# Optimization experiments

Measured on AMD Instinct MI355X. Metric: run time of the kernel, lower is better.

Reference implementation:

```python
import jax, jax.numpy as jnp
import numpy as np

N, IN, H, D, R, L, E, C = 100000, 128, 2, 64, 3, 2, 500000, 64
HID = H * D  # 128
EPS = 1e-5
NEG_SLOPE = 0.2


def setup_inputs() -> dict:
    key = jax.random.key(0)
    ks = jax.random.split(key, 11)
    s = 1.0 / np.sqrt(HID)
    return {
        "feat": jax.random.normal(ks[0], (N, IN), jnp.float32),
        "Ws": jax.random.normal(ks[1], (L, R, HID, HID), jnp.float32) * s,
        "als": jax.random.normal(ks[2], (L, R, H, D), jnp.float32) * s,
        "ars": jax.random.normal(ks[3], (L, R, H, D), jnp.float32) * s,
        "bs": jax.random.normal(ks[4], (L, R, HID), jnp.float32) * 0.01,
        "bn_w": jax.random.uniform(ks[5], (HID,), jnp.float32, 0.5, 1.5),
        "bn_b": jax.random.normal(ks[6], (HID,), jnp.float32) * 0.01,
        "clf_W": jax.random.normal(ks[7], (HID, C), jnp.float32) * s,
        "clf_b": jax.random.normal(ks[8], (C,), jnp.float32) * 0.01,
        "src": jax.random.randint(ks[9], (R, E), 0, N, jnp.int32),
        "dst": jax.random.randint(ks[10], (R, E), 0, N, jnp.int32),
    }


def _gat_rel(h, src, dst, W, al, ar, b):
    # DGL GATConv: feat [N,H,D]; e = leaky_relu(a_l.Wh_u + a_r.Wh_v);
    # alpha = softmax over in-edges of dst; out = scatter-sum(alpha*Wh_src) + bias
    feat = (h @ W).reshape(N, H, D)                     # [N,H,D]
    el = jnp.sum(feat * al, axis=-1)                    # [N,H]
    er = jnp.sum(feat * ar, axis=-1)                    # [N,H]
    e = jax.nn.leaky_relu(el[src] + er[dst], NEG_SLOPE) # [E,H]
    m = jax.ops.segment_max(e, dst, num_segments=N)     # [N,H]
    ex = jnp.exp(e - m[dst])
    ssum = jax.ops.segment_sum(ex, dst, num_segments=N)
    alpha = ex / ssum[dst]                              # [E,H]
    msg = feat[src] * alpha[:, :, None]                 # [E,H,D]
    out = jax.ops.segment_sum(msg, dst, num_segments=N) # [N,H,D]
    return out + b.reshape(1, H, D)


def reference(feat, Ws, als, ars, bs, bn_w, bn_b, clf_W, clf_b, src, dst):
    h = feat
    for l in range(L):
        acc = jnp.zeros((N, H, D), h.dtype)
        for r in range(R):  # HeteroGraphConv aggregate='sum' over relations
            acc = acc + _gat_rel(h, src[r], dst[r], Ws[l, r], als[l, r], ars[l, r], bs[l, r])
        h = jax.nn.relu(acc).reshape(N, HID)  # concat multihead agg
    # BatchNorm1d (training mode: batch stats, biased var) + Linear
    mu = jnp.mean(h, axis=0)
    var = jnp.var(h, axis=0)
    h = (h - mu) / jnp.sqrt(var + EPS) * bn_w + bn_b
    return h @ clf_W + clf_b
```

## Files before the change

kernel.cpp:

```cpp
#include <hip/hip_runtime.h>
#include <hip/hip_bf16.h>

#define N_NODES 100000
#define N_EDGES 500000
#define HID 128
#define NEG_SLOPE 0.2f
#define NB 98

typedef __attribute__((ext_vector_type(8))) short short8v;
typedef __attribute__((ext_vector_type(4))) short short4v;
typedef __attribute__((ext_vector_type(4))) float f32x4;

__device__ __forceinline__ short f2bf(float x) {
    union { float f; unsigned u; } v; v.f = x;
    unsigned r = v.u + 0x7fff + ((v.u >> 16) & 1);
    return (short)(r >> 16);
}
__device__ __forceinline__ float bflo(unsigned u) {
    union { unsigned x; float f; } c; c.x = u << 16; return c.f;
}
__device__ __forceinline__ float bfhi(unsigned u) {
    union { unsigned x; float f; } c; c.x = u & 0xffff0000u; return c.f;
}
__device__ __forceinline__ float bfs(short s) {
    union { unsigned x; float f; } c; c.x = ((unsigned)(unsigned short)s) << 16; return c.f;
}
__device__ __forceinline__ float asf(unsigned u) {
    union { unsigned x; float f; } c; c.x = u; return c.f;
}


__global__ __launch_bounds__(256) void k_bhist(const int* __restrict__ dst, int* __restrict__ bcnt) {
    int r = blockIdx.y, tid = threadIdx.x;
    int base = blockIdx.x * 4096;
    __shared__ int h[128];
    if (tid < 128) h[tid] = 0;
    __syncthreads();
    size_t eb = (size_t)r * N_EDGES;
    int lim = min(base + 4096, N_EDGES);
    for (int e = base + tid; e < lim; e += 256) atomicAdd(&h[dst[eb + e] >> 10], 1);
    __syncthreads();
    if (tid < NB && h[tid]) atomicAdd(&bcnt[r * NB + tid], h[tid]);
}

__global__ void k_bscan(const int* __restrict__ bcnt, int* __restrict__ bptr, int* __restrict__ bcur) {
    int r = blockIdx.x, lane = threadIdx.x;
    int carry = 0;
    for (int base = 0; base < NB; base += 64) {
        int i = base + lane;
        int c = (i < NB) ? bcnt[r * NB + i] : 0;
        int v = c;
        #pragma unroll
        for (int d = 1; d < 64; d <<= 1) { int t = __shfl_up(v, d); if (lane >= d) v += t; }
        int excl = carry + v - c;
        if (i < NB) { bptr[r * (NB + 1) + i] = excl; bcur[r * NB + i] = excl; }
        carry += __shfl(v, 63);
    }
    if (lane == 0) bptr[r * (NB + 1) + NB] = carry;
}

__global__ __launch_bounds__(256) void k_bin(const int* __restrict__ src, const int* __restrict__ dst,
                                             int* __restrict__ bcur, unsigned* __restrict__ ebin) {
    int r = blockIdx.y, tid = threadIdx.x;
    int base = blockIdx.x * 4096;
    __shared__ int cnt[128], incl[128], gb[128], wcur[128];
    __shared__ uint2 stage[4096];
    if (tid < 128) cnt[tid] = 0;
    __syncthreads();
    int myd[16], mys[16];
    size_t eb = (size_t)r * N_EDGES;
    #pragma unroll
    for (int i = 0; i < 16; i++) {
        int e = base + i * 256 + tid;
        if (e < N_EDGES) {
            int d = dst[eb + e];
            myd[i] = d; mys[i] = src[eb + e];
            atomicAdd(&cnt[d >> 10], 1);
        } else myd[i] = -1;
    }
    __syncthreads();
    if (tid < 128) incl[tid] = cnt[tid];
    __syncthreads();
    for (int d = 1; d < 128; d <<= 1) {
        int t = 0;
        if (tid < 128 && tid >= d) t = incl[tid - d];
        __syncthreads();
        if (tid < 128 && tid >= d) incl[tid] += t;
        __syncthreads();
    }
    if (tid < 128) {
        wcur[tid] = incl[tid] - cnt[tid];
        gb[tid] = (tid < NB && cnt[tid] > 0) ? atomicAdd(&bcur[r * NB + tid], cnt[tid]) : 0;
    }
    __syncthreads();
    #pragma unroll
    for (int i = 0; i < 16; i++) {
        if (myd[i] >= 0) {
            int bkt = myd[i] >> 10;
            int p = atomicAdd(&wcur[bkt], 1);
            stage[p] = make_uint2((unsigned)myd[i], (unsigned)mys[i]);
        }
    }
    __syncthreads();
    int tot = min(4096, N_EDGES - base);
    for (int i = tid; i < tot; i += 256) {
        uint2 u = stage[i];
        int bkt = (int)(u.x >> 10);
        int ex = incl[bkt] - cnt[bkt];
        ebin[eb + gb[bkt] + (i - ex)] = ((u.x & 1023u) << 17) | u.y;
    }
}

__global__ __launch_bounds__(256) void k_nhist(const unsigned* __restrict__ ebin,
                                               const int* __restrict__ bptr,
                                               int* __restrict__ rowptr) {
    int b = blockIdx.x, r = blockIdx.y, tid = threadIdx.x;
    __shared__ int cnt[1024];
    __shared__ int wsum[4];
    for (int i = tid; i < 1024; i += 256) cnt[i] = 0;
    __syncthreads();
    int es = bptr[r * (NB + 1) + b], ee = bptr[r * (NB + 1) + b + 1];
    size_t eb = (size_t)r * N_EDGES;
    for (int i = es + tid; i < ee; i += 256) atomicAdd(&cnt[(ebin[eb + i] >> 17) & 1023u], 1);
    __syncthreads();
    int b4 = tid * 4;
    int c0 = cnt[b4], c1 = cnt[b4 + 1], c2 = cnt[b4 + 2], c3 = cnt[b4 + 3];
    int ts = c0 + c1 + c2 + c3;
    int lane = tid & 63, wid = tid >> 6;
    int v = ts;
    #pragma unroll
    for (int d = 1; d < 64; d <<= 1) { int t = __shfl_up(v, d); if (lane >= d) v += t; }
    if (lane == 63) wsum[wid] = v;
    __syncthreads();
    int woff = 0;
    for (int w = 0; w < wid; w++) woff += wsum[w];
    int p = woff + v - ts;
    int node0 = b << 10;
    int rp = r * (N_NODES + 1);
    int nd;
    nd = node0 + b4;     if (nd < N_NODES) rowptr[rp + nd] = es + p; p += c0;
    nd = node0 + b4 + 1; if (nd < N_NODES) rowptr[rp + nd] = es + p; p += c1;
    nd = node0 + b4 + 2; if (nd < N_NODES) rowptr[rp + nd] = es + p; p += c2;
    nd = node0 + b4 + 3; if (nd < N_NODES) rowptr[rp + nd] = es + p;
    if (b == NB - 1 && tid == 0) rowptr[rp + N_NODES] = bptr[r * (NB + 1) + NB];
}

__global__ __launch_bounds__(256) void k_scat2(const unsigned* __restrict__ ebin,
                                               const int* __restrict__ bptr,
                                               const int* __restrict__ rowptr,
                                               int* __restrict__ csrc) {
    int b = blockIdx.x, r = blockIdx.y, tid = threadIdx.x;
    __shared__ int cnt[1024];
    __shared__ int rloc[1024];
    __shared__ int stage[8192];
    int node0 = b << 10;
    int rp = r * (N_NODES + 1);
    int rs = rowptr[rp + node0];
    for (int i = tid; i < 1024; i += 256) {
        cnt[i] = 0;
        int nd = node0 + i; if (nd > N_NODES) nd = N_NODES;
        rloc[i] = rowptr[rp + nd] - rs;
    }
    __syncthreads();
    int es = bptr[r * (NB + 1) + b], ee = bptr[r * (NB + 1) + b + 1];
    int sz = ee - es;
    size_t eb = (size_t)r * N_EDGES;
    if (sz <= 8192) {
        for (int i = es + tid; i < ee; i += 256) {
            unsigned u = ebin[eb + i];
            int dl = (int)((u >> 17) & 1023u);
            int rk = atomicAdd(&cnt[dl], 1);
            stage[rloc[dl] + rk] = (int)(u & 0x1FFFFu);
        }
        __syncthreads();
        for (int i = tid; i < sz; i += 256) csrc[eb + rs + i] = stage[i];
    } else {
        for (int i = es + tid; i < ee; i += 256) {
            unsigned u = ebin[eb + i];
            int dl = (int)((u >> 17) & 1023u);
            int rk = atomicAdd(&cnt[dl], 1);
            csrc[eb + rs + rloc[dl] + rk] = (int)(u & 0x1FFFFu);
        }
    }
}

__global__ void k_wprep(const float* __restrict__ Ws, short* __restrict__ Wt) {
    int i = blockIdx.x * blockDim.x + threadIdx.x;
    if (i < 6 * 16384) {
        int lr = i >> 14, rem = i & 16383, k = rem >> 7, col = rem & 127;
        Wt[lr * 16384 + col * 128 + (k ^ ((col & 7) << 3))] = f2bf(Ws[i]);
    }
}

__global__ void k_wprep2(const float* __restrict__ Wc, short* __restrict__ Wcb) {
    int i = blockIdx.x * blockDim.x + threadIdx.x;
    if (i < 8192) {
        int k = i >> 6, col = i & 63;
        Wcb[col * 128 + (k ^ ((col & 7) << 3))] = f2bf(Wc[i]);
    }
}

__global__ void k_cvt(const float* __restrict__ in, short* __restrict__ out, int n) {
    int i = blockIdx.x * blockDim.x + threadIdx.x;
    int stride = gridDim.x * blockDim.x;
    for (int base = i * 8; base < n; base += stride * 8) {
        float4 x = *(const float4*)(in + base);
        float4 y = *(const float4*)(in + base + 4);
        short8v o;
        o[0] = f2bf(x.x); o[1] = f2bf(x.y); o[2] = f2bf(x.z); o[3] = f2bf(x.w);
        o[4] = f2bf(y.x); o[5] = f2bf(y.y); o[6] = f2bf(y.z); o[7] = f2bf(y.w);
        *(short8v*)(out + base) = o;
    }
}

__global__ __launch_bounds__(256) void k_gemm3(const short* __restrict__ Abf,
                                               const short* __restrict__ Wt3,
                                               const float* __restrict__ al3,
                                               const float* __restrict__ ar3,
                                               short* __restrict__ featb,
                                               float4* __restrict__ elr,
                                               int nrows) {
    __shared__ __align__(16) short Wl[128 * 128];
    int tid = threadIdx.x;
    int lane = tid & 63, wid = tid >> 6;
    int q = lane >> 4, j = lane & 15;
    int rowbase = blockIdx.x * 128 + wid * 32;

    short8v a[2][4];
    #pragma unroll
    for (int rb = 0; rb < 2; rb++) {
        int row = rowbase + rb * 16 + j;
        const short* ap = Abf + (size_t)row * 128 + q * 8;
        bool ok = row < nrows;
        #pragma unroll
        for (int kk = 0; kk < 4; kk++)
            a[rb][kk] = ok ? *(const short8v*)(ap + kk * 32) : (short8v)0;
    }

    for (int cr = 0; cr < 3; cr++) {
        if (cr) __syncthreads();
        {
            const float4* srcv = (const float4*)(Wt3 + cr * 16384);
            float4* dstv = (float4*)Wl;
            #pragma unroll
            for (int i = 0; i < 8; i++) dstv[tid + i * 256] = srcv[tid + i * 256];
        }
        float alv[8], arv[8];
        #pragma unroll
        for (int cb = 0; cb < 8; cb++) {
            alv[cb] = al3[cr * 128 + cb * 16 + j];
            arv[cb] = ar3[cr * 128 + cb * 16 + j];
        }
        __syncthreads();

        f32x4 acc[2][8] = {};
        #pragma unroll
        for (int cb = 0; cb < 8; cb++) {
            int col = cb * 16 + j;
            const short* wp = Wl + col * 128;
            int sw = (col & 7) << 3;
            #pragma unroll
            for (int kk = 0; kk < 4; kk++) {
                short8v b = *(const short8v*)(wp + ((kk * 32 + q * 8) ^ sw));
                acc[0][cb] = __builtin_amdgcn_mfma_f32_16x16x32_bf16(a[0][kk], b, acc[0][cb], 0, 0, 0);
                acc[1][cb] = __builtin_amdgcn_mfma_f32_16x16x32_bf16(a[1][kk], b, acc[1][cb], 0, 0, 0);
            }
        }

        short* outB = featb + (size_t)cr * N_NODES * 128;
        #pragma unroll
        for (int rb = 0; rb < 2; rb++) {
            int row0 = rowbase + rb * 16 + q * 4;
            #pragma unroll
            for (int reg = 0; reg < 4; reg++) {
                int row = row0 + reg;
                if (row < nrows) {
                    short* op = outB + (size_t)row * 128 + j;
                    #pragma unroll
                    for (int cb = 0; cb < 8; cb++) op[cb * 16] = f2bf(acc[rb][cb][reg]);
                }
            }
        }

        float4* elro = elr + (size_t)cr * N_NODES;
        #pragma unroll
        for (int rb = 0; rb < 2; rb++) {
            float e0[4], e1[4], r0[4], r1[4];
            #pragma unroll
            for (int reg = 0; reg < 4; reg++) {
                float se0 = 0.f, se1 = 0.f, sr0 = 0.f, sr1 = 0.f;
                #pragma unroll
                for (int cb = 0; cb < 4; cb++) {
                    se0 += acc[rb][cb][reg] * alv[cb];
                    sr0 += acc[rb][cb][reg] * arv[cb];
                    se1 += acc[rb][cb + 4][reg] * alv[cb + 4];
                    sr1 += acc[rb][cb + 4][reg] * arv[cb + 4];
                }
                #pragma unroll
                for (int off = 1; off < 16; off <<= 1) {
                    se0 += __shfl_xor(se0, off);
                    se1 += __shfl_xor(se1, off);
                    sr0 += __shfl_xor(sr0, off);
                    sr1 += __shfl_xor(sr1, off);
                }
                e0[reg] = se0; e1[reg] = se1; r0[reg] = sr0; r1[reg] = sr1;
            }
            if (j < 4) {
                int row = rowbase + rb * 16 + q * 4 + j;
                if (row < nrows) {
                    float4 v;
                    v.x = j == 0 ? e0[0] : j == 1 ? e0[1] : j == 2 ? e0[2] : e0[3];
                    v.y = j == 0 ? e1[0] : j == 1 ? e1[1] : j == 2 ? e1[2] : e1[3];
                    v.z = j == 0 ? r0[0] : j == 1 ? r0[1] : j == 2 ? r0[2] : r0[3];
                    v.w = j == 0 ? r1[0] : j == 1 ? r1[1] : j == 2 ? r1[2] : r1[3];
                    elro[row] = v;
                }
            }
        }
    }
}

__global__ __launch_bounds__(256) void k_agg3(const short* __restrict__ feat,
                                              const float4* __restrict__ elr,
                                              const int* __restrict__ rowptr,
                                              const int* __restrict__ csrc,
                                              const float* __restrict__ bias,
                                              short* __restrict__ outB, int nrows) {
    int wid = threadIdx.x >> 6, lane = threadIdx.x & 63;
    int v = (blockIdx.x << 2) + wid;
    if (v >= nrows) return;
    int c0 = lane << 1;

    int beg[3], end[3], bc[3];
    #pragma unroll
    for (int r = 0; r < 3; r++) {
        beg[r] = rowptr[r * (N_NODES + 1) + v];
        end[r] = rowptr[r * (N_NODES + 1) + v + 1];
        bc[r] = min(64, end[r] - beg[r]);
    }
    float4 ev[3];
    #pragma unroll
    for (int r = 0; r < 3; r++) ev[r] = elr[(size_t)r * N_NODES + v];

    int sv[3]; unsigned pk[3];
    #pragma unroll
    for (int r = 0; r < 3; r++)
        sv[r] = (lane < end[r] - beg[r]) ? csrc[(size_t)r * N_EDGES + beg[r] + lane] : 0;
    #pragma unroll
    for (int r = 0; r < 3; r++) {
        float4 es = elr[(size_t)r * N_NODES + sv[r]];
        float e0 = es.x + ev[r].z; e0 = e0 >= 0.f ? e0 : NEG_SLOPE * e0;
        float e1 = es.y + ev[r].w; e1 = e1 >= 0.f ? e1 : NEG_SLOPE * e1;
        bool val = lane < (end[r] - beg[r]);
        float p0 = val ? __expf(e0) : 0.f;
        float p1 = val ? __expf(e1) : 0.f;
        pk[r] = ((unsigned)(unsigned short)f2bf(p0)) |
                (((unsigned)(unsigned short)f2bf(p1)) << 16);
    }

    float a0[3], a1[3], sp[3];
    bool lo = lane < 32;

    #pragma unroll
    for (int r = 0; r < 3; r++) {
        const short* fb = feat + (size_t)r * (N_NODES * 128);
        int nb = bc[r];
        float sA = 0.f, xa = 0.f, xb = 0.f, ya = 0.f, yb = 0.f;
        for (int j0 = 0; j0 < nb; j0 += 4) {
            int s0 = __builtin_amdgcn_readlane(sv[r], j0);
            int s1 = __builtin_amdgcn_readlane(sv[r], j0 + 1);
            int s2 = __builtin_amdgcn_readlane(sv[r], j0 + 2);
            int s3 = __builtin_amdgcn_readlane(sv[r], j0 + 3);
            unsigned b0 = (unsigned)__builtin_amdgcn_readlane((int)pk[r], j0);
            unsigned b1 = (unsigned)__builtin_amdgcn_readlane((int)pk[r], j0 + 1);
            unsigned b2 = (unsigned)__builtin_amdgcn_readlane((int)pk[r], j0 + 2);
            unsigned b3 = (unsigned)__builtin_amdgcn_readlane((int)pk[r], j0 + 3);
            unsigned u0 = *(const unsigned*)(fb + ((size_t)(unsigned)s0 << 7) + c0);
            unsigned u1 = *(const unsigned*)(fb + ((size_t)(unsigned)s1 << 7) + c0);
            unsigned u2 = *(const unsigned*)(fb + ((size_t)(unsigned)s2 << 7) + c0);
            unsigned u3 = *(const unsigned*)(fb + ((size_t)(unsigned)s3 << 7) + c0);
            float p0 = asf(lo ? (b0 << 16) : (b0 & 0xffff0000u));
            float p1 = asf(lo ? (b1 << 16) : (b1 & 0xffff0000u));
            float p2 = asf(lo ? (b2 << 16) : (b2 & 0xffff0000u));
            float p3 = asf(lo ? (b3 << 16) : (b3 & 0xffff0000u));
            sA += (p0 + p1) + (p2 + p3);
            xa += p0 * bflo(u0); xb += p0 * bfhi(u0);
            ya += p1 * bflo(u1); yb += p1 * bfhi(u1);
            xa += p2 * bflo(u2); xb += p2 * bfhi(u2);
            ya += p3 * bflo(u3); yb += p3 * bfhi(u3);
        }
        sp[r] = sA; a0[r] = xa + ya; a1[r] = xb + yb;
    }

    #pragma unroll
    for (int r = 0; r < 3; r++) {
        for (int base = beg[r] + 64; base < end[r]; base += 64) {
            int idx = base + lane;
            bool val = idx < end[r];
            int sv2 = val ? csrc[(size_t)r * N_EDGES + idx] : 0;
            float4 es = elr[(size_t)r * N_NODES + sv2];
            float e0 = es.x + ev[r].z; e0 = e0 >= 0.f ? e0 : NEG_SLOPE * e0;
            float e1 = es.y + ev[r].w; e1 = e1 >= 0.f ? e1 : NEG_SLOPE * e1;
            float q0v = val ? __expf(e0) : 0.f;
            float q1v = val ? __expf(e1) : 0.f;
            int bc2 = min(64, end[r] - base);
            for (int k = 0; k < bc2; k++) {
                int ss = __builtin_amdgcn_readlane(sv2, k);
                float q0 = asf((unsigned)__builtin_amdgcn_readlane((int)__float_as_uint(q0v), k));
                float q1 = asf((unsigned)__builtin_amdgcn_readlane((int)__float_as_uint(q1v), k));
                float pp = lo ? q0 : q1;
                unsigned u = *(const unsigned*)(feat + (size_t)r * N_NODES * 128 + ((size_t)ss << 7) + c0);
                sp[r] += pp;
                a0[r] += pp * bflo(u);
                a1[r] += pp * bfhi(u);
            }
        }
    }

    float t0 = bias[c0] + bias[128 + c0] + bias[256 + c0];
    float t1 = bias[c0 + 1] + bias[128 + c0 + 1] + bias[256 + c0 + 1];
    #pragma unroll
    for (int r = 0; r < 3; r++) {
        float inv = sp[r] > 0.f ? 1.0f / sp[r] : 0.f;
        t0 += a0[r] * inv;
        t1 += a1[r] * inv;
    }
    unsigned pko = ((unsigned)(unsigned short)f2bf(fmaxf(t0, 0.f))) |
                   (((unsigned)(unsigned short)f2bf(fmaxf(t1, 0.f))) << 16);
    *(unsigned*)(outB + (size_t)v * 128 + c0) = pko;
}

__global__ __launch_bounds__(256) void k_bnstat(const short* __restrict__ h,
                                                float* __restrict__ sums, int nrows) {
    int tid = threadIdx.x;
    int cg = tid & 15, rgrp = tid >> 4;
    float s[8] = {}, q[8] = {};
    for (int row = blockIdx.x * 16 + rgrp; row < nrows; row += gridDim.x * 16) {
        short8v u = *(const short8v*)(h + (size_t)row * 128 + cg * 8);
        #pragma unroll
        for (int i = 0; i < 8; i++) {
            float x = bfs(u[i]);
            s[i] += x; q[i] += x * x;
        }
    }
    __shared__ float ls[16][128];
    __shared__ float lq[16][128];
    #pragma unroll
    for (int i = 0; i < 8; i++) { ls[rgrp][cg * 8 + i] = s[i]; lq[rgrp][cg * 8 + i] = q[i]; }
    __syncthreads();
    int t = tid;
    if (t < 128) {
        float ts = 0.f, tq = 0.f;
        #pragma unroll
        for (int g = 0; g < 16; g++) { ts += ls[g][t]; tq += lq[g][t]; }
        atomicAdd(&sums[t], ts);
        atomicAdd(&sums[128 + t], tq);
    }
}

__global__ __launch_bounds__(256) void k_clf(const short* __restrict__ h,
                                             const float* __restrict__ sums,
                                             const float* __restrict__ bn_w,
                                             const float* __restrict__ bn_b,
                                             const short* __restrict__ Wcb,
                                             const float* __restrict__ cbias,
                                             float* __restrict__ out, int nrows) {
    __shared__ __align__(16) short Wl[64 * 128];
    __shared__ float2 bnp[128];
    int tid = threadIdx.x;
    {
        const float4* srcv = (const float4*)Wcb;
        float4* dstv = (float4*)Wl;
        #pragma unroll
        for (int i = 0; i < 4; i++) dstv[tid + i * 256] = srcv[tid + i * 256];
    }
    if (tid < 128) {
        float mu = sums[tid] / (float)nrows;
        float var = sums[128 + tid] / (float)nrows - mu * mu;
        float rs = rsqrtf(var + 1e-5f);
        float sc = bn_w[tid] * rs;
        bnp[tid] = make_float2(sc, bn_b[tid] - mu * sc);
    }
    __syncthreads();

    int lane = tid & 63, wid = tid >> 6;
    int q = lane >> 4, j = lane & 15;
    int rowbase = blockIdx.x * 128 + wid * 32;

    float cbv[4];
    #pragma unroll
    for (int cb = 0; cb < 4; cb++) cbv[cb] = cbias[cb * 16 + j];

    short8v a[2][4];
    #pragma unroll
    for (int rb = 0; rb < 2; rb++) {
        int row = rowbase + rb * 16 + j;
        bool ok = row < nrows;
        const short* hp = h + (size_t)row * 128 + q * 8;
        #pragma unroll
        for (int kk = 0; kk < 4; kk++) {
            short8v u = ok ? *(const short8v*)(hp + kk * 32) : (short8v)0;
            int k0 = kk * 32 + q * 8;
            short8v av;
            #pragma unroll
            for (int i = 0; i < 8; i++) {
                float2 bp = bnp[k0 + i];
                av[i] = f2bf(bfs(u[i]) * bp.x + bp.y);
            }
            a[rb][kk] = av;
        }
    }

    f32x4 acc[2][4] = {};
    #pragma unroll
    for (int cb = 0; cb < 4; cb++) {
        int col = cb * 16 + j;
        const short* wp = Wl + col * 128;
        int sw = (col & 7) << 3;
        #pragma unroll
        for (int kk = 0; kk < 4; kk++) {
            short8v b = *(const short8v*)(wp + ((kk * 32 + q * 8) ^ sw));
            acc[0][cb] = __builtin_amdgcn_mfma_f32_16x16x32_bf16(a[0][kk], b, acc[0][cb], 0, 0, 0);
            acc[1][cb] = __builtin_amdgcn_mfma_f32_16x16x32_bf16(a[1][kk], b, acc[1][cb], 0, 0, 0);
        }
    }

    #pragma unroll
    for (int rb = 0; rb < 2; rb++) {
        int row0 = rowbase + rb * 16 + q * 4;
        #pragma unroll
        for (int reg = 0; reg < 4; reg++) {
            int row = row0 + reg;
            if (row < nrows) {
                float* op = out + (size_t)row * 64 + j;
                #pragma unroll
                for (int cb = 0; cb < 4; cb++) op[cb * 16] = acc[rb][cb][reg] + cbv[cb];
            }
        }
    }
}


extern "C" void kernel_launch(void* const* d_in, const int* in_sizes, int n_in,
                              void* d_out, int out_size, void* d_ws, size_t ws_size,
                              hipStream_t stream) {
    (void)in_sizes; (void)n_in; (void)out_size; (void)ws_size;
    const float* feat_in = (const float*)d_in[0];
    const float* Ws      = (const float*)d_in[1];
    const float* als     = (const float*)d_in[2];
    const float* ars     = (const float*)d_in[3];
    const float* bs      = (const float*)d_in[4];
    const float* bn_w    = (const float*)d_in[5];
    const float* bn_b    = (const float*)d_in[6];
    const float* clf_W   = (const float*)d_in[7];
    const float* clf_b   = (const float*)d_in[8];
    const int*   src     = (const int*)d_in[9];
    const int*   dst     = (const int*)d_in[10];
    float* out = (float*)d_out;

    const int N = N_NODES, E = N_EDGES;
    char* p = (char*)d_ws;
    auto carve = [&](size_t bytes) { char* q = p; p += (bytes + 255) & ~255ULL; return q; };
    int*      bcnt   = (int*)carve((size_t)3 * NB * 4);
    int*      bptr   = (int*)carve((size_t)3 * (NB + 1) * 4);
    int*      bcur   = (int*)carve((size_t)3 * NB * 4);
    int*      rowptr = (int*)carve((size_t)3 * (N + 1) * 4);
    int*      csrc   = (int*)carve((size_t)3 * E * 4);
    unsigned* ebin   = (unsigned*)carve((size_t)3 * E * 4);
    float4*   elr    = (float4*)carve((size_t)3 * N * 16);
    float*    bnsum  = (float*)carve(256 * 4);
    short*    Wtg    = (short*)carve((size_t)6 * 16384 * 2);
    short*    Wcb    = (short*)carve((size_t)8192 * 2);
    short*    hA     = (short*)carve((size_t)N * 128 * 2);
    short*    hB     = (short*)carve((size_t)N * 128 * 2);
    short*    featb  = (short*)carve((size_t)3 * N * 128 * 2);

    k_wprep<<<(6 * 16384 + 255) / 256, 256, 0, stream>>>(Ws, Wtg);
    k_wprep2<<<32, 256, 0, stream>>>(clf_W, Wcb);
    k_cvt<<<2048, 256, 0, stream>>>(feat_in, hA, N * 128);

    hipMemsetAsync(bcnt, 0, (size_t)3 * NB * 4, stream);
    dim3 gchunk((E + 4095) / 4096, 3);
    k_bhist<<<gchunk, 256, 0, stream>>>(dst, bcnt);
    k_bscan<<<3, 64, 0, stream>>>(bcnt, bptr, bcur);
    k_bin<<<gchunk, 256, 0, stream>>>(src, dst, bcur, ebin);
    dim3 gbkt(NB, 3);
    k_nhist<<<gbkt, 256, 0, stream>>>(ebin, bptr, rowptr);
    k_scat2<<<gbkt, 256, 0, stream>>>(ebin, bptr, rowptr, csrc);

    int gq = (N + 3) / 4;
    for (int l = 0; l < 2; l++) {
        const short* hin = (l == 0) ? hA : hB;
        short* hout = (l == 0) ? hB : hA;
        k_gemm3<<<(N + 127) / 128, 256, 0, stream>>>(hin, Wtg + (size_t)l * 3 * 16384,
                                                     als + (size_t)l * 384, ars + (size_t)l * 384,
                                                     featb, elr, N);
        k_agg3<<<gq, 256, 0, stream>>>(featb, elr, rowptr, csrc,
                                       bs + (size_t)l * 384, hout, N);
    }

    hipMemsetAsync(bnsum, 0, 256 * 4, stream);
    k_bnstat<<<512, 256, 0, stream>>>(hA, bnsum, N);
    k_clf<<<(N + 127) / 128, 256, 0, stream>>>(hA, bnsum, bn_w, bn_b, Wcb, clf_b, out, N);
}
```

Before: 368.5 us.

## Split edge attention weights into a separate per-node pass before aggregation

```diff
diff --git a/kernel.cpp b/kernel.cpp
--- a/kernel.cpp
+++ b/kernel.cpp
@@ -320,8 +320,35 @@
     }
 }
 
+__global__ __launch_bounds__(256) void k_edgep(const float4* __restrict__ elr,
+                                               const int* __restrict__ rowptr,
+                                               const int* __restrict__ csrc,
+                                               unsigned* __restrict__ palpha,
+                                               float2* __restrict__ nsum,
+                                               int nrows) {
+    int r = blockIdx.y;
+    int v = blockIdx.x * 256 + threadIdx.x;
+    if (v >= nrows) return;
+    int beg = rowptr[r * (N_NODES + 1) + v], end = rowptr[r * (N_NODES + 1) + v + 1];
+    float4 ev = elr[(size_t)r * N_NODES + v];
+    size_t eb = (size_t)r * N_EDGES;
+    float s0 = 0.f, s1 = 0.f;
+    for (int i = beg; i < end; i++) {
+        int s = csrc[eb + i];
+        float4 es = elr[(size_t)r * N_NODES + s];
+        float e0 = es.x + ev.z; e0 = e0 >= 0.f ? e0 : NEG_SLOPE * e0;
+        float e1 = es.y + ev.w; e1 = e1 >= 0.f ? e1 : NEG_SLOPE * e1;
+        short b0 = f2bf(__expf(e0)), b1 = f2bf(__expf(e1));
+        palpha[eb + i] = ((unsigned)(unsigned short)b0) | (((unsigned)(unsigned short)b1) << 16);
+        s0 += bfs(b0); s1 += bfs(b1);
+    }
+    nsum[(size_t)r * N_NODES + v] = make_float2(s0 > 0.f ? 1.0f / s0 : 0.f,
+                                                s1 > 0.f ? 1.0f / s1 : 0.f);
+}
+
 __global__ __launch_bounds__(256) void k_agg3(const short* __restrict__ feat,
-                                              const float4* __restrict__ elr,
+                                              const unsigned* __restrict__ palpha,
+                                              const float2* __restrict__ nsum,
                                               const int* __restrict__ rowptr,
                                               const int* __restrict__ csrc,
                                               const float* __restrict__ bias,
@@ -330,6 +357,7 @@
     int v = (blockIdx.x << 2) + wid;
     if (v >= nrows) return;
     int c0 = lane << 1;
+    bool lo = lane < 32;
 
     int beg[3], end[3], bc[3];
     #pragma unroll
@@ -338,34 +366,23 @@
         end[r] = rowptr[r * (N_NODES + 1) + v + 1];
         bc[r] = min(64, end[r] - beg[r]);
     }
-    float4 ev[3];
-    #pragma unroll
-    for (int r = 0; r < 3; r++) ev[r] = elr[(size_t)r * N_NODES + v];
 
     int sv[3]; unsigned pk[3];
     #pragma unroll
-    for (int r = 0; r < 3; r++)
-        sv[r] = (lane < end[r] - beg[r]) ? csrc[(size_t)r * N_EDGES + beg[r] + lane] : 0;
-    #pragma unroll
     for (int r = 0; r < 3; r++) {
-        float4 es = elr[(size_t)r * N_NODES + sv[r]];
-        float e0 = es.x + ev[r].z; e0 = e0 >= 0.f ? e0 : NEG_SLOPE * e0;
-        float e1 = es.y + ev[r].w; e1 = e1 >= 0.f ? e1 : NEG_SLOPE * e1;
-        bool val = lane < (end[r] - beg[r]);
-        float p0 = val ? __expf(e0) : 0.f;
-        float p1 = val ? __expf(e1) : 0.f;
-        pk[r] = ((unsigned)(unsigned short)f2bf(p0)) |
-                (((unsigned)(unsigned short)f2bf(p1)) << 16);
-    }
-
-    float a0[3], a1[3], sp[3];
-    bool lo = lane < 32;
+        bool val = lane < end[r] - beg[r];
+        size_t idx = (size_t)r * N_EDGES + beg[r] + lane;
+        sv[r] = val ? csrc[idx] : 0;
+        pk[r] = val ? palpha[idx] : 0u;
+    }
+
+    float a0[3], a1[3];
 
     #pragma unroll
     for (int r = 0; r < 3; r++) {
         const short* fb = feat + (size_t)r * (N_NODES * 128);
         int nb = bc[r];
-        float sA = 0.f, xa = 0.f, xb = 0.f, ya = 0.f, yb = 0.f;
+        float xa = 0.f, xb = 0.f, ya = 0.f, yb = 0.f;
         for (int j0 = 0; j0 < nb; j0 += 4) {
             int s0 = __builtin_amdgcn_readlane(sv[r], j0);
             int s1 = __builtin_amdgcn_readlane(sv[r], j0 + 1);
@@ -383,34 +400,28 @@
             float p1 = asf(lo ? (b1 << 16) : (b1 & 0xffff0000u));
             float p2 = asf(lo ? (b2 << 16) : (b2 & 0xffff0000u));
             float p3 = asf(lo ? (b3 << 16) : (b3 & 0xffff0000u));
-            sA += (p0 + p1) + (p2 + p3);
             xa += p0 * bflo(u0); xb += p0 * bfhi(u0);
             ya += p1 * bflo(u1); yb += p1 * bfhi(u1);
             xa += p2 * bflo(u2); xb += p2 * bfhi(u2);
             ya += p3 * bflo(u3); yb += p3 * bfhi(u3);
         }
-        sp[r] = sA; a0[r] = xa + ya; a1[r] = xb + yb;
+        a0[r] = xa + ya; a1[r] = xb + yb;
     }
 
     #pragma unroll
     for (int r = 0; r < 3; r++) {
+        const short* fb = feat + (size_t)r * (N_NODES * 128);
         for (int base = beg[r] + 64; base < end[r]; base += 64) {
             int idx = base + lane;
             bool val = idx < end[r];
             int sv2 = val ? csrc[(size_t)r * N_EDGES + idx] : 0;
-            float4 es = elr[(size_t)r * N_NODES + sv2];
-            float e0 = es.x + ev[r].z; e0 = e0 >= 0.f ? e0 : NEG_SLOPE * e0;
-            float e1 = es.y + ev[r].w; e1 = e1 >= 0.f ? e1 : NEG_SLOPE * e1;
-            float q0v = val ? __expf(e0) : 0.f;
-            float q1v = val ? __expf(e1) : 0.f;
+            unsigned pk2 = val ? palpha[(size_t)r * N_EDGES + idx] : 0u;
             int bc2 = min(64, end[r] - base);
             for (int k = 0; k < bc2; k++) {
                 int ss = __builtin_amdgcn_readlane(sv2, k);
-                float q0 = asf((unsigned)__builtin_amdgcn_readlane((int)__float_as_uint(q0v), k));
-                float q1 = asf((unsigned)__builtin_amdgcn_readlane((int)__float_as_uint(q1v), k));
-                float pp = lo ? q0 : q1;
-                unsigned u = *(const unsigned*)(feat + (size_t)r * N_NODES * 128 + ((size_t)ss << 7) + c0);
-                sp[r] += pp;
+                unsigned pb = (unsigned)__builtin_amdgcn_readlane((int)pk2, k);
+                float pp = asf(lo ? (pb << 16) : (pb & 0xffff0000u));
+                unsigned u = *(const unsigned*)(fb + ((size_t)(unsigned)ss << 7) + c0);
                 a0[r] += pp * bflo(u);
                 a1[r] += pp * bfhi(u);
             }
@@ -421,9 +432,10 @@
     float t1 = bias[c0 + 1] + bias[128 + c0 + 1] + bias[256 + c0 + 1];
     #pragma unroll
     for (int r = 0; r < 3; r++) {
-        float inv = sp[r] > 0.f ? 1.0f / sp[r] : 0.f;
-        t0 += a0[r] * inv;
-        t1 += a1[r] * inv;
+        float2 iv = nsum[(size_t)r * N_NODES + v];
+        float ii = lo ? iv.x : iv.y;
+        t0 += a0[r] * ii;
+        t1 += a1[r] * ii;
     }
     unsigned pko = ((unsigned)(unsigned short)f2bf(fmaxf(t0, 0.f))) |
                    (((unsigned)(unsigned short)f2bf(fmaxf(t1, 0.f))) << 16);
@@ -567,6 +579,8 @@
     int*      rowptr = (int*)carve((size_t)3 * (N + 1) * 4);
     int*      csrc   = (int*)carve((size_t)3 * E * 4);
     unsigned* ebin   = (unsigned*)carve((size_t)3 * E * 4);
+    unsigned* palpha = (unsigned*)carve((size_t)3 * E * 4);
+    float2*   nsum   = (float2*)carve((size_t)3 * N * 8);
     float4*   elr    = (float4*)carve((size_t)3 * N * 16);
     float*    bnsum  = (float*)carve(256 * 4);
     short*    Wtg    = (short*)carve((size_t)6 * 16384 * 2);
@@ -589,13 +603,15 @@
     k_scat2<<<gbkt, 256, 0, stream>>>(ebin, bptr, rowptr, csrc);
 
     int gq = (N + 3) / 4;
+    dim3 gep((N + 255) / 256, 3);
     for (int l = 0; l < 2; l++) {
         const short* hin = (l == 0) ? hA : hB;
         short* hout = (l == 0) ? hB : hA;
         k_gemm3<<<(N + 127) / 128, 256, 0, stream>>>(hin, Wtg + (size_t)l * 3 * 16384,
                                                      als + (size_t)l * 384, ars + (size_t)l * 384,
                                                      featb, elr, N);
-        k_agg3<<<gq, 256, 0, stream>>>(featb, elr, rowptr, csrc,
+        k_edgep<<<gep, 256, 0, stream>>>(elr, rowptr, csrc, palpha, nsum, N);
+        k_agg3<<<gq, 256, 0, stream>>>(featb, palpha, nsum, rowptr, csrc,
                                        bs + (size_t)l * 384, hout, N);
     }
 
```

Result: slower. 394.7 us (+7.1%).
